# Optimization experiments

Hardware: AMD Instinct MI355X
Metric: run time of the kernel (lower is better)

## Reference

```python
import jax, jax.numpy as jnp
import numpy as np

# Dimensions: B graphs, N padded nodes/graph, E edges/graph, D feature dim,
# H attention heads (concat=False -> head average), L stacked GAT layers.
B, N, E, D, H, L = 64, 1024, 16384, 300, 5, 2
NEG_SLOPE = 0.2   # PyG GATConv default negative_slope
LN_EPS = 1e-5


def setup_inputs() -> dict:
    key = jax.random.key(0)
    ks = jax.random.split(key, 6)
    t2 = jax.random.normal(ks[0], (B, N, D), dtype=jnp.float32)
    edge_index = jax.random.randint(ks[1], (B, 2, E), 0, N, dtype=jnp.int32)
    gnn_mask = jnp.zeros((B, N), dtype=bool)  # True = padded node
    # Per-layer GATConv parameters (heads=5, concat=False -> out dim D)
    W = jax.random.normal(ks[2], (L, D, H * D), dtype=jnp.float32) * 0.05
    att_src = jax.random.normal(ks[3], (L, H, D), dtype=jnp.float32) * 0.05
    att_dst = jax.random.normal(ks[4], (L, H, D), dtype=jnp.float32) * 0.05
    bias = jnp.zeros((L, D), dtype=jnp.float32)
    # Shared LayerNorm (single nn.LayerNorm reused after every layer)
    ln_gamma = jnp.ones((D,), dtype=jnp.float32)
    ln_beta = jnp.zeros((D,), dtype=jnp.float32)
    return {"t2": t2, "edge_index": edge_index, "gnn_mask": gnn_mask,
            "W": W, "att_src": att_src, "att_dst": att_dst, "bias": bias,
            "ln_gamma": ln_gamma, "ln_beta": ln_beta}


def _layernorm(x, g, b):
    mu = jnp.mean(x, axis=-1, keepdims=True)
    var = jnp.mean(jnp.square(x - mu), axis=-1, keepdims=True)
    return (x - mu) * jax.lax.rsqrt(var + LN_EPS) * g + b


def _gat_conv(x, src, dst, mask, Wl, a_src, a_dst, bl):
    """Single-graph GATConv: x[N,D], src/dst[E], mask[N] (True=padded)."""
    n = x.shape[0]
    h = (x @ Wl).reshape(n, H, D)                       # [N,H,D] projected per head
    a_s = jnp.einsum('nhd,hd->nh', h, a_src)            # [N,H]
    a_d = jnp.einsum('nhd,hd->nh', h, a_dst)            # [N,H]
    e = jax.nn.leaky_relu(a_s[src] + a_d[dst], NEG_SLOPE)  # [E,H] edge scores
    # drop messages originating from padded nodes
    e = jnp.where(mask[src][:, None], -1e9, e)
    # scatter-softmax over incoming edges of each destination node
    m = jax.ops.segment_max(e, dst, num_segments=n)     # [N,H]
    ex = jnp.exp(e - m[dst])
    den = jax.ops.segment_sum(ex, dst, num_segments=n)  # [N,H]
    alpha = ex / (den[dst] + 1e-16)                     # [E,H]
    # scatter-add aggregation of head-weighted messages
    out = jax.ops.segment_sum(alpha[:, :, None] * h[src], dst, num_segments=n)
    return out.mean(axis=1) + bl                        # concat=False: head mean, [N,D]


def reference(t2, edge_index, gnn_mask, W, att_src, att_dst, bias, ln_gamma, ln_beta):
    x = t2
    for l in range(L):
        conv = lambda xg, ei, mg: _gat_conv(xg, ei[0], ei[1], mg,
                                            W[l], att_src[l], att_dst[l], bias[l])
        x = jax.vmap(conv)(x, edge_index, gnn_mask)     # batch over graphs
        x = _layernorm(jax.nn.gelu(x), ln_gamma, ln_beta)  # GELU then shared LayerNorm
    return x
```

## Files before the change

kernel.cpp:

```cpp
#include <hip/hip_runtime.h>
#include <cstdint>
#include <cstddef>

typedef unsigned short u16;
typedef short short8 __attribute__((ext_vector_type(8)));
typedef __bf16 bf16x8 __attribute__((ext_vector_type(8)));
typedef float f32x4 __attribute__((ext_vector_type(4)));

#define BB 64
#define NNODE 1024
#define EDGES 16384
#define DIM 300
#define HEADS 5
#define LAYERS 2
#define K_PAD 320
#define N_PAD 1536
#define BM 128
#define BK 32

__device__ __forceinline__ u16 f32_to_bf16(float f) {
    union { float f; uint32_t u; } v; v.f = f;
    uint32_t u = v.u;
    uint32_t r = u + 0x7fffu + ((u >> 16) & 1u);
    return (u16)(r >> 16);
}
__device__ __forceinline__ float bf16_to_f32(u16 h) {
    union { uint32_t u; float f; } v; v.u = ((uint32_t)h) << 16;
    return v.f;
}

__global__ __launch_bounds__(256) void csr_build(const int* __restrict__ ei,
                                                 int* __restrict__ offs,
                                                 int* __restrict__ csr_src) {
    int b = blockIdx.x;
    const int* src = ei + (size_t)b * 2 * EDGES;
    const int* dst = src + EDGES;
    __shared__ int cnt[NNODE];
    __shared__ int grp[256];
    int t = threadIdx.x;
    for (int i = t; i < NNODE; i += 256) cnt[i] = 0;
    __syncthreads();
    for (int e = t; e < EDGES; e += 256) atomicAdd(&cnt[dst[e]], 1);
    __syncthreads();
    int c0 = cnt[4 * t + 0], c1 = cnt[4 * t + 1], c2 = cnt[4 * t + 2], c3 = cnt[4 * t + 3];
    grp[t] = c0 + c1 + c2 + c3;
    __syncthreads();
    for (int off = 1; off < 256; off <<= 1) {
        int v = (t >= off) ? grp[t - off] : 0;
        __syncthreads();
        grp[t] += v;
        __syncthreads();
    }
    int base = (t == 0) ? 0 : grp[t - 1];
    int o0 = base, o1 = o0 + c0, o2 = o1 + c1, o3 = o2 + c2;
    cnt[4 * t + 0] = o0; cnt[4 * t + 1] = o1; cnt[4 * t + 2] = o2; cnt[4 * t + 3] = o3;
    int* ob = offs + b * (NNODE + 1);
    ob[4 * t + 0] = o0; ob[4 * t + 1] = o1; ob[4 * t + 2] = o2; ob[4 * t + 3] = o3;
    if (t == 0) ob[NNODE] = EDGES;
    __syncthreads();
    for (int e = t; e < EDGES; e += 256) {
        int d = dst[e];
        int pos = atomicAdd(&cnt[d], 1);
        csr_src[(size_t)b * EDGES + pos] = src[e];
    }
}

__global__ __launch_bounds__(256) void split_w_all(const float* __restrict__ W,
                                                   u16* __restrict__ hi, u16* __restrict__ lo) {
    int i = blockIdx.x * 256 + threadIdx.x;
    int k = i % K_PAD;
    int rem = i / K_PAD;
    int n = rem % N_PAD;
    int l = rem / N_PAD;
    float v = (k < DIM && n < HEADS * DIM)
                  ? W[((size_t)l * DIM + k) * (HEADS * DIM) + n]
                  : 0.f;
    u16 h = f32_to_bf16(v);
    hi[i] = h;
    lo[i] = f32_to_bf16(v - bf16_to_f32(h));
}

__global__ __launch_bounds__(256) void pad_x(const float* __restrict__ X,
                                             float* __restrict__ Xp) {
    size_t i = (size_t)blockIdx.x * 256 + threadIdx.x;
    int k = (int)(i % K_PAD);
    size_t row = i / K_PAD;
    Xp[i] = (k < DIM) ? X[row * DIM + k] : 0.f;
}

__device__ __forceinline__ f32x4 mfma16(short8 a, short8 b, f32x4 c) {
    return __builtin_amdgcn_mfma_f32_16x16x32_bf16(
        __builtin_bit_cast(bf16x8, a), __builtin_bit_cast(bf16x8, b), c, 0, 0, 0);
}

__global__ __launch_bounds__(256) void gemm_split(const float* __restrict__ Xp,
                                                  const u16* __restrict__ Bhi,
                                                  const u16* __restrict__ Blo,
                                                  u16* __restrict__ Hout) {
    __shared__ __align__(16) short lds[3][BM][BK];
    int t = threadIdx.x;
    int m0 = blockIdx.x * BM, n0 = blockIdx.y * BM;
    int lane = t & 63, w = t >> 6, wr = w >> 1, wc = w & 1;
    int lrow = lane & 15, kg = lane >> 4;

    const u16* gWh = Bhi + (size_t)n0 * K_PAD;
    const u16* gWl = Blo + (size_t)n0 * K_PAD;

    f32x4 acc[4][4] = {};

    for (int k0 = 0; k0 < K_PAD; k0 += BK) {
        __syncthreads();
#pragma unroll
        for (int i = 0; i < 2; i++) {
            int chunk = t + (i << 8);
            int row = chunk >> 2, g = chunk & 3;
            const float* src = &Xp[(size_t)(m0 + row) * K_PAD + k0 + g * 8];
            f32x4 v0 = *(const f32x4*)src;
            f32x4 v1 = *(const f32x4*)(src + 4);
            short8 h8;
#pragma unroll
            for (int j = 0; j < 8; j++) {
                float f = (j < 4) ? v0[j] : v1[j - 4];
                h8[j] = (short)f32_to_bf16(f);
            }
            int gsw = (g ^ ((row >> 1) & 3)) * 8;
            *(short8*)&lds[0][row][gsw] = h8;
        }
#pragma unroll
        for (int i = 0; i < 4; i++) {
            int chunk = t + ((i & 1) << 8);
            int row = chunk >> 2, g = chunk & 3;
            int gsw = (g ^ ((row >> 1) & 3)) * 8;
            const u16* gs = (i < 2) ? gWh : gWl;
            short* ls = (i < 2) ? &lds[1][row][gsw] : &lds[2][row][gsw];
            *(short8*)ls = *(const short8*)&gs[(size_t)row * K_PAD + k0 + g * 8];
        }
        __syncthreads();

        short8 ah[4], bh[4], bl[4];
#pragma unroll
        for (int f = 0; f < 4; f++) {
            int ra = wr * 64 + f * 16 + lrow;
            int sa = (kg ^ ((ra >> 1) & 3)) * 8;
            ah[f] = *(const short8*)&lds[0][ra][sa];
            int rb = wc * 64 + f * 16 + lrow;
            int sb = (kg ^ ((rb >> 1) & 3)) * 8;
            bh[f] = *(const short8*)&lds[1][rb][sb];
            bl[f] = *(const short8*)&lds[2][rb][sb];
        }
#pragma unroll
        for (int fm = 0; fm < 4; fm++)
#pragma unroll
            for (int fn = 0; fn < 4; fn++) {
                acc[fm][fn] = mfma16(ah[fm], bl[fn], acc[fm][fn]);
                acc[fm][fn] = mfma16(ah[fm], bh[fn], acc[fm][fn]);
            }
    }

#pragma unroll
    for (int fm = 0; fm < 4; fm++)
#pragma unroll
        for (int fn = 0; fn < 4; fn++)
#pragma unroll
            for (int i = 0; i < 4; i++) {
                int row = m0 + wr * 64 + fm * 16 + (lane >> 4) * 4 + i;
                int col = n0 + wc * 64 + fn * 16 + (lane & 15);
                Hout[(size_t)row * N_PAD + col] = f32_to_bf16(acc[fm][fn][i]);
            }
}

__global__ __launch_bounds__(256) void head_dots(const u16* __restrict__ Hb,
                                                 const float* __restrict__ att_s,
                                                 const float* __restrict__ att_d,
                                                 float* __restrict__ a_s,
                                                 float* __restrict__ a_d) {
    int node = blockIdx.x * 4 + (threadIdx.x >> 6);
    int lane = threadIdx.x & 63;
    const u16* row = Hb + (size_t)node * N_PAD;
#pragma unroll
    for (int hd = 0; hd < HEADS; hd++) {
        float ss = 0.f, sd = 0.f;
        for (int c = hd * DIM + lane; c < (hd + 1) * DIM; c += 64) {
            float hv = bf16_to_f32(row[c]);
            ss += hv * att_s[c];
            sd += hv * att_d[c];
        }
#pragma unroll
        for (int o = 32; o > 0; o >>= 1) {
            ss += __shfl_down(ss, o);
            sd += __shfl_down(sd, o);
        }
        if (lane == 0) {
            a_s[(size_t)node * HEADS + hd] = ss;
            a_d[(size_t)node * HEADS + hd] = sd;
        }
    }
}

__global__ __launch_bounds__(320) void agg_kernel(const u16* __restrict__ Hb,
                                                  const float* __restrict__ a_s,
                                                  const float* __restrict__ a_d_arr,
                                                  const int* __restrict__ offs,
                                                  const int* __restrict__ csr_src,
                                                  const unsigned char* __restrict__ mask,
                                                  const float* __restrict__ bias_l,
                                                  const float* __restrict__ gamma,
                                                  const float* __restrict__ beta,
                                                  int graph0,
                                                  float* __restrict__ out,
                                                  int ldo, int do_pad) {
    int nb = blockIdx.x;
    int xcd = nb & 7;
    int j = nb >> 3;
    int b = xcd + 8 * (j >> 10);
    int n = j & 1023;
    int node = b * NNODE + n;
    int gb = graph0 + b;
    int t = threadIdx.x;
    int wave = t >> 6, lane = t & 63;

    __shared__ float s_p[64][HEADS];
    __shared__ int   s_srcs[64];
    __shared__ float s_scale[HEADS];
    __shared__ float s_den[HEADS];
    __shared__ float s_part[2][HEADS];

    int off0 = offs[gb * (NNODE + 1) + n];
    int deg = offs[gb * (NNODE + 1) + n + 1] - off0;
    const int* slist = csr_src + (size_t)gb * EDGES + off0;

    float adh = a_d_arr[(size_t)node * HEADS + wave];
    const float* as_g = a_s + (size_t)b * NNODE * HEADS;
    const unsigned char* mk_g = mask + (size_t)gb * NNODE;
    const u16* hbase = Hb + (size_t)b * NNODE * N_PAD + t;

    float m_run = -1e30f, den_run = 0.f;
    float acc[HEADS] = {0.f, 0.f, 0.f, 0.f, 0.f};

    for (int c0 = 0; c0 < deg; c0 += 64) {
        int cn = min(64, deg - c0);
        if (t < cn) s_srcs[t] = slist[c0 + t];
        __syncthreads();

        float sc = -1e30f;
        if (lane < cn) {
            int s = s_srcs[lane];
            float v = as_g[s * HEADS + wave] + adh;
            v = (v >= 0.f) ? v : 0.2f * v;
            if (mk_g[s]) v = -1e9f;
            sc = v;
        }
        float cm = sc;
#pragma unroll
        for (int o = 32; o > 0; o >>= 1) cm = fmaxf(cm, __shfl_xor(cm, o));
        float m_new = fmaxf(m_run, cm);
        float scale = (m_run <= -1e29f) ? 0.f : __expf(m_run - m_new);
        float p = (lane < cn) ? __expf(sc - m_new) : 0.f;
        float ds = p;
#pragma unroll
        for (int o = 32; o > 0; o >>= 1) ds += __shfl_xor(ds, o);
        den_run = den_run * scale + ds;
        m_run = m_new;
        s_p[lane][wave] = p;
        if (lane == 0) s_scale[wave] = scale;
        __syncthreads();

        if (t < DIM) {
#pragma unroll
            for (int h = 0; h < HEADS; h++) acc[h] *= s_scale[h];
            int e = 0;
            for (; e + 2 <= cn; e += 2) {
                const u16* h0 = hbase + (size_t)s_srcs[e] * N_PAD;
                const u16* h1 = hbase + (size_t)s_srcs[e + 1] * N_PAD;
                float q00 = s_p[e][0], q01 = s_p[e][1], q02 = s_p[e][2],
                      q03 = s_p[e][3], q04 = s_p[e][4];
                float q10 = s_p[e + 1][0], q11 = s_p[e + 1][1], q12 = s_p[e + 1][2],
                      q13 = s_p[e + 1][3], q14 = s_p[e + 1][4];
                acc[0] += q00 * bf16_to_f32(h0[0 * DIM]) + q10 * bf16_to_f32(h1[0 * DIM]);
                acc[1] += q01 * bf16_to_f32(h0[1 * DIM]) + q11 * bf16_to_f32(h1[1 * DIM]);
                acc[2] += q02 * bf16_to_f32(h0[2 * DIM]) + q12 * bf16_to_f32(h1[2 * DIM]);
                acc[3] += q03 * bf16_to_f32(h0[3 * DIM]) + q13 * bf16_to_f32(h1[3 * DIM]);
                acc[4] += q04 * bf16_to_f32(h0[4 * DIM]) + q14 * bf16_to_f32(h1[4 * DIM]);
            }
            if (e < cn) {
                const u16* h0 = hbase + (size_t)s_srcs[e] * N_PAD;
                acc[0] += s_p[e][0] * bf16_to_f32(h0[0 * DIM]);
                acc[1] += s_p[e][1] * bf16_to_f32(h0[1 * DIM]);
                acc[2] += s_p[e][2] * bf16_to_f32(h0[2 * DIM]);
                acc[3] += s_p[e][3] * bf16_to_f32(h0[3 * DIM]);
                acc[4] += s_p[e][4] * bf16_to_f32(h0[4 * DIM]);
            }
        }
        __syncthreads();
    }

    if (lane == 0) s_den[wave] = den_run + 1e-16f;
    __syncthreads();

    float g = 0.f;
    if (t < DIM) {
        float x = 0.f;
#pragma unroll
        for (int h = 0; h < HEADS; h++) x += acc[h] / s_den[h];
        x = x * 0.2f + bias_l[t];
        float u = 0.7978845608028654f * (x + 0.044715f * x * x * x);
        g = 0.5f * x * (1.f + tanhf(u));
    }
    float sum = g;
#pragma unroll
    for (int o = 32; o > 0; o >>= 1) sum += __shfl_xor(sum, o);
    if (lane == 0) s_part[0][wave] = sum;
    __syncthreads();
    float mu = (s_part[0][0] + s_part[0][1] + s_part[0][2] + s_part[0][3] + s_part[0][4])
               * (1.f / DIM);
    float dv = (t < DIM) ? (g - mu) : 0.f;
    float sq = dv * dv;
#pragma unroll
    for (int o = 32; o > 0; o >>= 1) sq += __shfl_xor(sq, o);
    if (lane == 0) s_part[1][wave] = sq;
    __syncthreads();
    float var = (s_part[1][0] + s_part[1][1] + s_part[1][2] + s_part[1][3] + s_part[1][4])
                * (1.f / DIM);
    if (t < DIM) {
        float y = dv * rsqrtf(var + 1e-5f) * gamma[t] + beta[t];
        out[(size_t)node * ldo + t] = y;
    } else if (do_pad) {
        out[(size_t)node * ldo + t] = 0.f;
    }
}

extern "C" void kernel_launch(void* const* d_in, const int* in_sizes, int n_in,
                              void* d_out, int out_size, void* d_ws, size_t ws_size,
                              hipStream_t stream) {
    const float* t2      = (const float*)d_in[0];
    const int*   ei      = (const int*)d_in[1];
    const unsigned char* mask = (const unsigned char*)d_in[2];
    const float* W       = (const float*)d_in[3];
    const float* att_src = (const float*)d_in[4];
    const float* att_dst = (const float*)d_in[5];
    const float* bias    = (const float*)d_in[6];
    const float* gamma   = (const float*)d_in[7];
    const float* beta    = (const float*)d_in[8];

    auto aln = [](size_t b) { return (b + 255) & ~(size_t)255; };
    auto need = [&](int CB) {
        size_t s = 0;
        s += aln((size_t)LAYERS * N_PAD * K_PAD * 2) * 2;
        s += aln((size_t)CB * NNODE * K_PAD * 4);
        s += aln((size_t)CB * NNODE * N_PAD * 2);
        s += aln((size_t)CB * NNODE * HEADS * 4) * 2;
        s += aln((size_t)BB * (NNODE + 1) * 4);
        s += aln((size_t)BB * EDGES * 4);
        return s;
    };
    int CB = 32;
    if (ws_size == 0) CB = 8;
    else while (CB > 8 && need(CB) > ws_size) CB >>= 1;
    const int MC = CB * NNODE;

    char* p = (char*)d_ws;
    auto alloc = [&](size_t bytes) {
        char* r = p;
        p += (bytes + 255) & ~(size_t)255;
        return r;
    };
    u16* Wthi = (u16*)alloc((size_t)LAYERS * N_PAD * K_PAD * 2);
    u16* Wtlo = (u16*)alloc((size_t)LAYERS * N_PAD * K_PAD * 2);
    float* Xpad = (float*)alloc((size_t)MC * K_PAD * 4);
    u16* Hb   = (u16*)alloc((size_t)MC * N_PAD * 2);
    float* a_s = (float*)alloc((size_t)MC * HEADS * 4);
    float* a_d = (float*)alloc((size_t)MC * HEADS * 4);
    int* offs  = (int*)alloc((size_t)BB * (NNODE + 1) * 4);
    int* csr   = (int*)alloc((size_t)BB * EDGES * 4);

    csr_build<<<BB, 256, 0, stream>>>(ei, offs, csr);
    split_w_all<<<(LAYERS * N_PAD * K_PAD) / 256, 256, 0, stream>>>(W, Wthi, Wtlo);

    for (int g0 = 0; g0 < BB; g0 += CB) {
        pad_x<<<(MC * K_PAD) / 256, 256, 0, stream>>>(t2 + (size_t)g0 * NNODE * DIM, Xpad);
        for (int l = 0; l < LAYERS; l++) {
            dim3 gg(MC / BM, N_PAD / BM);
            gemm_split<<<gg, 256, 0, stream>>>(Xpad,
                                               Wthi + (size_t)l * N_PAD * K_PAD,
                                               Wtlo + (size_t)l * N_PAD * K_PAD, Hb);
            head_dots<<<MC / 4, 256, 0, stream>>>(Hb, att_src + (size_t)l * HEADS * DIM,
                                                  att_dst + (size_t)l * HEADS * DIM, a_s, a_d);
            if (l == LAYERS - 1) {
                agg_kernel<<<MC, 320, 0, stream>>>(Hb, a_s, a_d, offs, csr, mask,
                                                   bias + (size_t)l * DIM, gamma, beta,
                                                   g0, (float*)d_out + (size_t)g0 * NNODE * DIM,
                                                   DIM, 0);
            } else {
                agg_kernel<<<MC, 320, 0, stream>>>(Hb, a_s, a_d, offs, csr, mask,
                                                   bias + (size_t)l * DIM, gamma, beta,
                                                   g0, Xpad, K_PAD, 1);
            }
        }
    }
}
```

Before: 1.522 ms.

## Store activations as bf16 and restructure aggregation to per-head wave gathers

```diff
diff --git a/kernel.cpp b/kernel.cpp
--- a/kernel.cpp
+++ b/kernel.cpp
@@ -80,12 +80,13 @@
     lo[i] = f32_to_bf16(v - bf16_to_f32(h));
 }
 
-__global__ __launch_bounds__(256) void pad_x(const float* __restrict__ X,
-                                             float* __restrict__ Xp) {
+__global__ __launch_bounds__(256) void pad_x_bf16(const float* __restrict__ X,
+                                                  u16* __restrict__ Xb) {
     size_t i = (size_t)blockIdx.x * 256 + threadIdx.x;
     int k = (int)(i % K_PAD);
     size_t row = i / K_PAD;
-    Xp[i] = (k < DIM) ? X[row * DIM + k] : 0.f;
+    float v = (k < DIM) ? X[row * DIM + k] : 0.f;
+    Xb[i] = f32_to_bf16(v);
 }
 
 __device__ __forceinline__ f32x4 mfma16(short8 a, short8 b, f32x4 c) {
@@ -93,16 +94,17 @@
         __builtin_bit_cast(bf16x8, a), __builtin_bit_cast(bf16x8, b), c, 0, 0, 0);
 }
 
-__global__ __launch_bounds__(256) void gemm_split(const float* __restrict__ Xp,
-                                                  const u16* __restrict__ Bhi,
-                                                  const u16* __restrict__ Blo,
-                                                  u16* __restrict__ Hout) {
+__global__ __launch_bounds__(256) void gemm_bf16(const u16* __restrict__ A,
+                                                 const u16* __restrict__ Bhi,
+                                                 const u16* __restrict__ Blo,
+                                                 u16* __restrict__ Hout) {
     __shared__ __align__(16) short lds[3][BM][BK];
     int t = threadIdx.x;
     int m0 = blockIdx.x * BM, n0 = blockIdx.y * BM;
     int lane = t & 63, w = t >> 6, wr = w >> 1, wc = w & 1;
     int lrow = lane & 15, kg = lane >> 4;
 
+    const u16* gA  = A   + (size_t)m0 * K_PAD;
     const u16* gWh = Bhi + (size_t)n0 * K_PAD;
     const u16* gWl = Blo + (size_t)n0 * K_PAD;
 
@@ -111,28 +113,15 @@
     for (int k0 = 0; k0 < K_PAD; k0 += BK) {
         __syncthreads();
 #pragma unroll
-        for (int i = 0; i < 2; i++) {
-            int chunk = t + (i << 8);
-            int row = chunk >> 2, g = chunk & 3;
-            const float* src = &Xp[(size_t)(m0 + row) * K_PAD + k0 + g * 8];
-            f32x4 v0 = *(const f32x4*)src;
-            f32x4 v1 = *(const f32x4*)(src + 4);
-            short8 h8;
-#pragma unroll
-            for (int j = 0; j < 8; j++) {
-                float f = (j < 4) ? v0[j] : v1[j - 4];
-                h8[j] = (short)f32_to_bf16(f);
-            }
-            int gsw = (g ^ ((row >> 1) & 3)) * 8;
-            *(short8*)&lds[0][row][gsw] = h8;
-        }
-#pragma unroll
-        for (int i = 0; i < 4; i++) {
+        for (int i = 0; i < 6; i++) {
             int chunk = t + ((i & 1) << 8);
             int row = chunk >> 2, g = chunk & 3;
             int gsw = (g ^ ((row >> 1) & 3)) * 8;
-            const u16* gs = (i < 2) ? gWh : gWl;
-            short* ls = (i < 2) ? &lds[1][row][gsw] : &lds[2][row][gsw];
+            const u16* gs;
+            short* ls;
+            if (i < 2)      { gs = gA;  ls = &lds[0][row][gsw]; }
+            else if (i < 4) { gs = gWh; ls = &lds[1][row][gsw]; }
+            else            { gs = gWl; ls = &lds[2][row][gsw]; }
             *(short8*)ls = *(const short8*)&gs[(size_t)row * K_PAD + k0 + g * 8];
         }
         __syncthreads();
@@ -207,8 +196,9 @@
                                                   const float* __restrict__ gamma,
                                                   const float* __restrict__ beta,
                                                   int graph0,
-                                                  float* __restrict__ out,
-                                                  int ldo, int do_pad) {
+                                                  float* __restrict__ out_f32,
+                                                  u16* __restrict__ out_bf16,
+                                                  int ldo) {
     int nb = blockIdx.x;
     int xcd = nb & 7;
     int j = nb >> 3;
@@ -217,37 +207,34 @@
     int node = b * NNODE + n;
     int gb = graph0 + b;
     int t = threadIdx.x;
-    int wave = t >> 6, lane = t & 63;
-
-    __shared__ float s_p[64][HEADS];
-    __shared__ int   s_srcs[64];
-    __shared__ float s_scale[HEADS];
-    __shared__ float s_den[HEADS];
+    int w = t >> 6, lane = t & 63;
+
+    __shared__ __align__(16) float s_acc[HEADS][304];
     __shared__ float s_part[2][HEADS];
 
     int off0 = offs[gb * (NNODE + 1) + n];
     int deg = offs[gb * (NNODE + 1) + n + 1] - off0;
     const int* slist = csr_src + (size_t)gb * EDGES + off0;
 
-    float adh = a_d_arr[(size_t)node * HEADS + wave];
+    float adh = a_d_arr[(size_t)node * HEADS + w];
     const float* as_g = a_s + (size_t)b * NNODE * HEADS;
     const unsigned char* mk_g = mask + (size_t)gb * NNODE;
-    const u16* hbase = Hb + (size_t)b * NNODE * N_PAD + t;
+    const u16* hrow0 = Hb + (size_t)b * NNODE * N_PAD + w * DIM;
 
     float m_run = -1e30f, den_run = 0.f;
-    float acc[HEADS] = {0.f, 0.f, 0.f, 0.f, 0.f};
+    float acc0[4] = {0.f, 0.f, 0.f, 0.f};
+    float acc1[4] = {0.f, 0.f, 0.f, 0.f};
 
     for (int c0 = 0; c0 < deg; c0 += 64) {
         int cn = min(64, deg - c0);
-        if (t < cn) s_srcs[t] = slist[c0 + t];
-        __syncthreads();
-
+
+        int s_v = 0;
         float sc = -1e30f;
         if (lane < cn) {
-            int s = s_srcs[lane];
-            float v = as_g[s * HEADS + wave] + adh;
+            s_v = slist[c0 + lane];
+            float v = as_g[s_v * HEADS + w] + adh;
             v = (v >= 0.f) ? v : 0.2f * v;
-            if (mk_g[s]) v = -1e9f;
+            if (mk_g[s_v]) v = -1e9f;
             sc = v;
         }
         float cm = sc;
@@ -261,55 +248,54 @@
         for (int o = 32; o > 0; o >>= 1) ds += __shfl_xor(ds, o);
         den_run = den_run * scale + ds;
         m_run = m_new;
-        s_p[lane][wave] = p;
-        if (lane == 0) s_scale[wave] = scale;
-        __syncthreads();
-
-        if (t < DIM) {
-#pragma unroll
-            for (int h = 0; h < HEADS; h++) acc[h] *= s_scale[h];
-            int e = 0;
-            for (; e + 2 <= cn; e += 2) {
-                const u16* h0 = hbase + (size_t)s_srcs[e] * N_PAD;
-                const u16* h1 = hbase + (size_t)s_srcs[e + 1] * N_PAD;
-                float q00 = s_p[e][0], q01 = s_p[e][1], q02 = s_p[e][2],
-                      q03 = s_p[e][3], q04 = s_p[e][4];
-                float q10 = s_p[e + 1][0], q11 = s_p[e + 1][1], q12 = s_p[e + 1][2],
-                      q13 = s_p[e + 1][3], q14 = s_p[e + 1][4];
-                acc[0] += q00 * bf16_to_f32(h0[0 * DIM]) + q10 * bf16_to_f32(h1[0 * DIM]);
-                acc[1] += q01 * bf16_to_f32(h0[1 * DIM]) + q11 * bf16_to_f32(h1[1 * DIM]);
-                acc[2] += q02 * bf16_to_f32(h0[2 * DIM]) + q12 * bf16_to_f32(h1[2 * DIM]);
-                acc[3] += q03 * bf16_to_f32(h0[3 * DIM]) + q13 * bf16_to_f32(h1[3 * DIM]);
-                acc[4] += q04 * bf16_to_f32(h0[4 * DIM]) + q14 * bf16_to_f32(h1[4 * DIM]);
-            }
-            if (e < cn) {
-                const u16* h0 = hbase + (size_t)s_srcs[e] * N_PAD;
-                acc[0] += s_p[e][0] * bf16_to_f32(h0[0 * DIM]);
-                acc[1] += s_p[e][1] * bf16_to_f32(h0[1 * DIM]);
-                acc[2] += s_p[e][2] * bf16_to_f32(h0[2 * DIM]);
-                acc[3] += s_p[e][3] * bf16_to_f32(h0[3 * DIM]);
-                acc[4] += s_p[e][4] * bf16_to_f32(h0[4 * DIM]);
-            }
-        }
-        __syncthreads();
-    }
-
-    if (lane == 0) s_den[wave] = den_run + 1e-16f;
+#pragma unroll
+        for (int q = 0; q < 4; q++) { acc0[q] *= scale; acc1[q] *= scale; }
+
+        uint32_t p_u = __builtin_bit_cast(uint32_t, p);
+        for (int e = 0; e < cn; e++) {
+            int se = __builtin_amdgcn_readlane(s_v, e);
+            float a = __builtin_bit_cast(float,
+                          (uint32_t)__builtin_amdgcn_readlane((int)p_u, e));
+            const u16* r = hrow0 + (size_t)se * N_PAD;
+            {
+                unsigned long long v8 = *(const unsigned long long*)(r + 4 * lane);
+                uint32_t lo = (uint32_t)v8, hi = (uint32_t)(v8 >> 32);
+                acc0[0] += a * __builtin_bit_cast(float, lo << 16);
+                acc0[1] += a * __builtin_bit_cast(float, lo & 0xffff0000u);
+                acc0[2] += a * __builtin_bit_cast(float, hi << 16);
+                acc0[3] += a * __builtin_bit_cast(float, hi & 0xffff0000u);
+            }
+            if (lane < 11) {
+                unsigned long long v8 = *(const unsigned long long*)(r + 256 + 4 * lane);
+                uint32_t lo = (uint32_t)v8, hi = (uint32_t)(v8 >> 32);
+                acc1[0] += a * __builtin_bit_cast(float, lo << 16);
+                acc1[1] += a * __builtin_bit_cast(float, lo & 0xffff0000u);
+                acc1[2] += a * __builtin_bit_cast(float, hi << 16);
+                acc1[3] += a * __builtin_bit_cast(float, hi & 0xffff0000u);
+            }
+        }
+    }
+
+    float inv = 0.2f / (den_run + 1e-16f);
+    f32x4 st0 = { acc0[0] * inv, acc0[1] * inv, acc0[2] * inv, acc0[3] * inv };
+    *(f32x4*)&s_acc[w][4 * lane] = st0;
+    if (lane < 11) {
+        f32x4 st1 = { acc1[0] * inv, acc1[1] * inv, acc1[2] * inv, acc1[3] * inv };
+        *(f32x4*)&s_acc[w][256 + 4 * lane] = st1;
+    }
     __syncthreads();
 
     float g = 0.f;
     if (t < DIM) {
-        float x = 0.f;
-#pragma unroll
-        for (int h = 0; h < HEADS; h++) x += acc[h] / s_den[h];
-        x = x * 0.2f + bias_l[t];
+        float x = s_acc[0][t] + s_acc[1][t] + s_acc[2][t] + s_acc[3][t] + s_acc[4][t]
+                  + bias_l[t];
         float u = 0.7978845608028654f * (x + 0.044715f * x * x * x);
         g = 0.5f * x * (1.f + tanhf(u));
     }
     float sum = g;
 #pragma unroll
     for (int o = 32; o > 0; o >>= 1) sum += __shfl_xor(sum, o);
-    if (lane == 0) s_part[0][wave] = sum;
+    if (lane == 0) s_part[0][w] = sum;
     __syncthreads();
     float mu = (s_part[0][0] + s_part[0][1] + s_part[0][2] + s_part[0][3] + s_part[0][4])
                * (1.f / DIM);
@@ -317,15 +303,20 @@
     float sq = dv * dv;
 #pragma unroll
     for (int o = 32; o > 0; o >>= 1) sq += __shfl_xor(sq, o);
-    if (lane == 0) s_part[1][wave] = sq;
+    if (lane == 0) s_part[1][w] = sq;
     __syncthreads();
     float var = (s_part[1][0] + s_part[1][1] + s_part[1][2] + s_part[1][3] + s_part[1][4])
                 * (1.f / DIM);
-    if (t < DIM) {
+    if (out_bf16) {
+        if (t < DIM) {
+            float y = dv * rsqrtf(var + 1e-5f) * gamma[t] + beta[t];
+            out_bf16[(size_t)node * ldo + t] = f32_to_bf16(y);
+        } else {
+            out_bf16[(size_t)node * ldo + t] = 0;
+        }
+    } else if (t < DIM) {
         float y = dv * rsqrtf(var + 1e-5f) * gamma[t] + beta[t];
-        out[(size_t)node * ldo + t] = y;
-    } else if (do_pad) {
-        out[(size_t)node * ldo + t] = 0.f;
+        out_f32[(size_t)node * ldo + t] = y;
     }
 }
 
@@ -346,7 +337,7 @@
     auto need = [&](int CB) {
         size_t s = 0;
         s += aln((size_t)LAYERS * N_PAD * K_PAD * 2) * 2;
-        s += aln((size_t)CB * NNODE * K_PAD * 4);
+        s += aln((size_t)CB * NNODE * K_PAD * 2);
         s += aln((size_t)CB * NNODE * N_PAD * 2);
         s += aln((size_t)CB * NNODE * HEADS * 4) * 2;
         s += aln((size_t)BB * (NNODE + 1) * 4);
@@ -366,7 +357,7 @@
     };
     u16* Wthi = (u16*)alloc((size_t)LAYERS * N_PAD * K_PAD * 2);
     u16* Wtlo = (u16*)alloc((size_t)LAYERS * N_PAD * K_PAD * 2);
-    float* Xpad = (float*)alloc((size_t)MC * K_PAD * 4);
+    u16* Xb   = (u16*)alloc((size_t)MC * K_PAD * 2);
     u16* Hb   = (u16*)alloc((size_t)MC * N_PAD * 2);
     float* a_s = (float*)alloc((size_t)MC * HEADS * 4);
     float* a_d = (float*)alloc((size_t)MC * HEADS * 4);
@@ -377,24 +368,24 @@
     split_w_all<<<(LAYERS * N_PAD * K_PAD) / 256, 256, 0, stream>>>(W, Wthi, Wtlo);
 
     for (int g0 = 0; g0 < BB; g0 += CB) {
-        pad_x<<<(MC * K_PAD) / 256, 256, 0, stream>>>(t2 + (size_t)g0 * NNODE * DIM, Xpad);
+        pad_x_bf16<<<(MC * K_PAD) / 256, 256, 0, stream>>>(t2 + (size_t)g0 * NNODE * DIM, Xb);
         for (int l = 0; l < LAYERS; l++) {
             dim3 gg(MC / BM, N_PAD / BM);
-            gemm_split<<<gg, 256, 0, stream>>>(Xpad,
-                                               Wthi + (size_t)l * N_PAD * K_PAD,
-                                               Wtlo + (size_t)l * N_PAD * K_PAD, Hb);
+            gemm_bf16<<<gg, 256, 0, stream>>>(Xb,
+                                              Wthi + (size_t)l * N_PAD * K_PAD,
+                                              Wtlo + (size_t)l * N_PAD * K_PAD, Hb);
             head_dots<<<MC / 4, 256, 0, stream>>>(Hb, att_src + (size_t)l * HEADS * DIM,
                                                   att_dst + (size_t)l * HEADS * DIM, a_s, a_d);
             if (l == LAYERS - 1) {
                 agg_kernel<<<MC, 320, 0, stream>>>(Hb, a_s, a_d, offs, csr, mask,
                                                    bias + (size_t)l * DIM, gamma, beta,
                                                    g0, (float*)d_out + (size_t)g0 * NNODE * DIM,
-                                                   DIM, 0);
+                                                   nullptr, DIM);
             } else {
                 agg_kernel<<<MC, 320, 0, stream>>>(Hb, a_s, a_d, offs, csr, mask,
                                                    bias + (size_t)l * DIM, gamma, beta,
-                                                   g0, Xpad, K_PAD, 1);
-            }
-        }
-    }
-}
+                                                   g0, nullptr, Xb, K_PAD);
+            }
+        }
+    }
+}
```

After: 1.534 ms. About the same (+0.8%).
